# Optimization experiments

Hardware: AMD Instinct MI355X
Metric: run time of the kernel (lower is better)

Reference implementation:

```python
import jax, jax.numpy as jnp
import numpy as np

N, M, B = 1024, 8192, 8192  # W: [N, M], x: [B, N]
BLOCK = 32


def activation_quant(x):
    # per-tensor symmetric int8 fake-quant with STE
    scale = 127.0 / jnp.clip(jnp.max(jnp.abs(x)), 1e-8, None)
    x_q = jnp.clip(jnp.round(x * scale), -128.0, 127.0) / scale
    return x + jax.lax.stop_gradient(x_q - x)


def weight_quant_q2_k(w, block_size=BLOCK):
    # blockwise 2-bit quant with top-2 outliers kept at 4-bit, STE
    shape = w.shape
    wf = w.reshape(-1)
    n = wf.shape[0]
    pad = (-n) % block_size
    wf = jnp.pad(wf, (0, pad))
    blocks = wf.reshape(-1, block_size)
    scales = jnp.clip(jnp.max(jnp.abs(blocks), axis=1, keepdims=True), 1e-8, None)
    nb = blocks / scales
    k = min(2, block_size)
    _, top_idx = jax.lax.top_k(jnp.abs(nb), k)
    rows = jnp.arange(nb.shape[0])[:, None]
    top_mask = jnp.zeros(nb.shape, dtype=bool).at[rows, top_idx].set(True)
    q4 = jnp.round(nb * 7.0) / 7.0
    abs_nb = jnp.abs(nb)
    q2 = jnp.sign(nb) * jnp.where(abs_nb > 0.66, 1.0, 1.0 / 3.0)
    q = jnp.where(top_mask, q4, q2) * scales
    w_q = q.reshape(-1)[:n].reshape(shape)
    return w + jax.lax.stop_gradient(w_q - w)


def setup_inputs() -> dict:
    key = jax.random.key(0)
    k1, k2, k3 = jax.random.split(key, 3)
    x = jax.random.normal(k1, (B, N), dtype=jnp.float32)
    W = jax.random.normal(k2, (N, M), dtype=jnp.float32) / np.float32(np.sqrt(M))
    b = jax.random.normal(k3, (N,), dtype=jnp.float32)
    idx = jnp.arange(M // 2, dtype=jnp.int32)            # expanded (quantized) columns
    idx_comp = jnp.arange(M // 2, M, dtype=jnp.int32)    # continuous columns
    return {"x": x, "W": W, "b": b, "idx": idx, "idx_comp": idx_comp}


def reference(x, W, b, idx, idx_comp):
    W_exp_q = weight_quant_q2_k(jnp.take(W, idx, axis=1))   # [N, M/2]
    W_cont = jnp.take(W, idx_comp, axis=1)                  # [N, M/2]
    hidden_exp = activation_quant(x) @ W_exp_q              # [B, M/2]
    hidden_cont = x @ W_cont                                # [B, M/2]
    hidden = (jnp.zeros((x.shape[0], M), dtype=x.dtype)
              .at[:, idx].set(hidden_exp)
              .at[:, idx_comp].set(hidden_cont))            # scatter back to [B, M]
    h_exp = activation_quant(hidden[:, idx])
    out = jax.nn.relu(h_exp @ W_exp_q.T + hidden[:, idx_comp] @ W_cont.T + b)
    return out
```

## Files before the change

kernel.cpp:

```cpp
#include <hip/hip_runtime.h>
#include <hip/hip_bf16.h>
#include <cstdint>


using bf16x8 = __attribute__((ext_vector_type(8))) __bf16;
using f32x4  = __attribute__((ext_vector_type(4))) float;

typedef const __attribute__((address_space(1))) void g_void;
typedef __attribute__((address_space(3))) void l_void;

__device__ __forceinline__ void gload16(const void* g, void* l) {
  __builtin_amdgcn_global_load_lds((g_void*)g, (l_void*)l, 16, 0, 0);
}

__device__ __forceinline__ ushort f2bf(float f) {
  union { float f; unsigned u; } c; c.f = f;
  unsigned r = c.u + 0x7FFFu + ((c.u >> 16) & 1u);
  return (ushort)(r >> 16);
}
__device__ __forceinline__ float bf2f(ushort u) {
  union { unsigned u; float f; } c; c.u = ((unsigned)u) << 16;
  return c.f;
}

__global__ void prep_wa_kernel(const float* __restrict__ W,
                               const float4* __restrict__ x,
                               ushort* __restrict__ Wq,
                               ushort* __restrict__ WqT,
                               ushort* __restrict__ Wcb,
                               unsigned* __restrict__ amax_bits) {
  const int bidx = blockIdx.x;
  const int tid = threadIdx.x;

  if (bidx < 1024) {
    __shared__ __align__(16) ushort tile[64][72];
    const int rt = bidx >> 6;
    const int ct = bidx & 63;
    const int r0 = rt * 64, c0 = ct * 64;
    const int e = tid & 31;
    const int hw = tid >> 5;
    #pragma unroll
    for (int it = 0; it < 16; ++it) {
      const int g = it * 8 + hw;
      const int row = g >> 1;
      const int cg = (g & 1) * 32;
      const float w = W[(size_t)(r0 + row) * 8192 + c0 + cg + e];
      float aw = fabsf(w);
      float m = aw;
      #pragma unroll
      for (int d = 1; d <= 16; d <<= 1) m = fmaxf(m, __shfl_xor(m, d));
      int idx = (aw == m) ? e : 32;
      #pragma unroll
      for (int d = 1; d <= 16; d <<= 1) idx = min(idx, __shfl_xor(idx, d));
      const int i1 = idx;
      float a2 = (e == i1) ? -1.f : aw;
      float m2 = a2;
      #pragma unroll
      for (int d = 1; d <= 16; d <<= 1) m2 = fmaxf(m2, __shfl_xor(m2, d));
      int idx2 = (a2 == m2) ? e : 32;
      #pragma unroll
      for (int d = 1; d <= 16; d <<= 1) idx2 = min(idx2, __shfl_xor(idx2, d));
      const int i2 = idx2;

      const float scale = fmaxf(m, 1e-8f);
      const float nb = w / scale;
      float q;
      if (e == i1 || e == i2) {
        q = rintf(nb * 7.f) / 7.f;
      } else {
        float s = (nb > 0.f) ? 1.f : ((nb < 0.f) ? -1.f : 0.f);
        q = s * ((fabsf(nb) > 0.66f) ? 1.f : (1.f / 3.f));
      }
      const ushort qb = f2bf(q * scale);
      Wq[(size_t)(r0 + row) * 4096 + c0 + cg + e] = qb;
      tile[cg + e][row] = qb;
    }
    __syncthreads();
    const int c = tid >> 2;
    const int q4 = (tid & 3) * 16;
    uint4 v0 = *(const uint4*)&tile[c][q4];
    uint4 v1 = *(const uint4*)&tile[c][q4 + 8];
    *(uint4*)(WqT + (size_t)(c0 + c) * 1024 + r0 + q4) = v0;
    *(uint4*)(WqT + (size_t)(c0 + c) * 1024 + r0 + q4 + 8) = v1;
  } else if (bidx < 5120) {
    const int u = (bidx - 1024) * 256 + tid;
    const int row = u >> 10;
    const int c4 = u & 1023;
    float4 v = *(const float4*)(W + (size_t)row * 8192 + 4096 + c4 * 4);
    ushort4 o;
    o.x = f2bf(v.x); o.y = f2bf(v.y); o.z = f2bf(v.z); o.w = f2bf(v.w);
    *(ushort4*)(Wcb + (size_t)row * 4096 + c4 * 4) = o;
  } else {
    float m = 0.f;
    const int base = (bidx - 5120) * 256 + tid;
    const int stride = 2048 * 256;
    for (int i = base; i < 8192 * 1024 / 4; i += stride) {
      float4 v = x[i];
      m = fmaxf(m, fmaxf(fmaxf(fabsf(v.x), fabsf(v.y)),
                         fmaxf(fabsf(v.z), fabsf(v.w))));
    }
    #pragma unroll
    for (int off = 32; off > 0; off >>= 1) m = fmaxf(m, __shfl_down(m, off));
    __shared__ float wm[4];
    int lane = tid & 63, wave = tid >> 6;
    if (lane == 0) wm[wave] = m;
    __syncthreads();
    if (tid == 0) {
      float r = fmaxf(fmaxf(wm[0], wm[1]), fmaxf(wm[2], wm[3]));
      atomicMax(amax_bits, __float_as_uint(r));
    }
  }
}

__global__ void prep_x_kernel(const float4* __restrict__ x,
                              const unsigned* __restrict__ amax_bits,
                              uint4* __restrict__ xq, uint4* __restrict__ xbf) {
  const float amax = fmaxf(__uint_as_float(*amax_bits), 1e-8f);
  const float scale = 127.f / amax;
  const int base = blockIdx.x * 256 + threadIdx.x;
  const int stride = 2048 * 256;
  const int n8 = 8192 * 1024 / 8;
  for (int i = base; i < n8; i += stride) {
    float4 a = x[i * 2], b = x[i * 2 + 1];
    float v[8] = {a.x, a.y, a.z, a.w, b.x, b.y, b.z, b.w};
    unsigned qw[4], bw[4];
    #pragma unroll
    for (int j = 0; j < 4; ++j) {
      float q0 = fminf(fmaxf(rintf(v[2 * j] * scale), -128.f), 127.f) / scale;
      float q1 = fminf(fmaxf(rintf(v[2 * j + 1] * scale), -128.f), 127.f) / scale;
      qw[j] = (unsigned)f2bf(q0) | ((unsigned)f2bf(q1) << 16);
      bw[j] = (unsigned)f2bf(v[2 * j]) | ((unsigned)f2bf(v[2 * j + 1]) << 16);
    }
    xq[i] = make_uint4(qw[0], qw[1], qw[2], qw[3]);
    xbf[i] = make_uint4(bw[0], bw[1], bw[2], bw[3]);
  }
}

__global__ __launch_bounds__(256, 2) void gemm1_kernel(
    const ushort* __restrict__ Wcb,
    ushort* __restrict__ G,
    const ushort* __restrict__ Aq, const ushort* __restrict__ BT,
    ushort* __restrict__ Hexp, unsigned* __restrict__ amax_bits) {
  __shared__ __align__(16) ushort As[2][128 * 32];
  __shared__ __align__(16) ushort Bs[2][128 * 32];
  __shared__ float wredmax[4];

  const int bidx = blockIdx.x;
  const int tid = threadIdx.x;
  const int lane = tid & 63, wave = tid >> 6;
  const int l15 = lane & 15, quad = lane >> 4;
  const int wm = (wave >> 1) << 6, wn = (wave & 1) << 6;
  const int sel = (quad ^ ((l15 >> 1) & 3)) * 8;
  const int scs = ((tid & 3) ^ ((tid >> 3) & 3)) * 8;

  ushort* Asl0 = As[0] + tid * 8; ushort* Asl1 = As[1] + tid * 8;
  ushort* Bsl0 = Bs[0] + tid * 8; ushort* Bsl1 = Bs[1] + tid * 8;

  f32x4 acc[4][4];
  #pragma unroll
  for (int i = 0; i < 4; ++i)
    #pragma unroll
    for (int j = 0; j < 4; ++j) acc[i][j] = (f32x4){0.f, 0.f, 0.f, 0.f};

  if (bidx < 64) {
    const int gy = bidx >> 3, gx = bidx & 7;
    const int i0 = gy * 128, j0 = gx * 128;
    const ushort* Ag = Wcb + (size_t)(i0 + (tid >> 2)) * 4096 + scs;
    const ushort* Bg = Wcb + (size_t)(j0 + (tid >> 2)) * 4096 + scs;
    for (int k0 = 0; k0 < 4096; k0 += 64) {
      __syncthreads();
      gload16(Ag + k0, Asl0);
      gload16(Ag + (size_t)64 * 4096 + k0, Asl0 + 64 * 32);
      gload16(Bg + k0, Bsl0);
      gload16(Bg + (size_t)64 * 4096 + k0, Bsl0 + 64 * 32);
      gload16(Ag + k0 + 32, Asl1);
      gload16(Ag + (size_t)64 * 4096 + k0 + 32, Asl1 + 64 * 32);
      gload16(Bg + k0 + 32, Bsl1);
      gload16(Bg + (size_t)64 * 4096 + k0 + 32, Bsl1 + 64 * 32);
      __syncthreads();
      #pragma unroll
      for (int p = 0; p < 2; ++p) {
        bf16x8 af[4], bfr[4];
        #pragma unroll
        for (int i = 0; i < 4; ++i)
          af[i] = *(const bf16x8*)&As[p][(wm + i * 16 + l15) * 32 + sel];
        #pragma unroll
        for (int j = 0; j < 4; ++j)
          bfr[j] = *(const bf16x8*)&Bs[p][(wn + j * 16 + l15) * 32 + sel];
        #pragma unroll
        for (int i = 0; i < 4; ++i)
          #pragma unroll
          for (int j = 0; j < 4; ++j)
            acc[i][j] = __builtin_amdgcn_mfma_f32_16x16x32_bf16(af[i], bfr[j], acc[i][j], 0, 0, 0);
      }
    }
    const int row0 = i0 + wm + quad * 4;
    const int col0 = j0 + wn + l15;
    #pragma unroll
    for (int i = 0; i < 4; ++i)
      #pragma unroll
      for (int j = 0; j < 4; ++j)
        #pragma unroll
        for (int r = 0; r < 4; ++r)
          G[(size_t)(row0 + i * 16 + r) * 1024 + (col0 + j * 16)] = f2bf(acc[i][j][r]);
    return;
  }

  const int l = bidx - 64;
  const int xcd = l & 7;
  const int s = l >> 3;
  const int t = (xcd << 2) | (s >> 6);
  const int u = s & 63;
  const int bx = ((t & 3) << 3) | (u & 7);
  const int by = ((t >> 2) << 3) | (u >> 3);

  const ushort* Ag = Aq + (size_t)(by * 128 + (tid >> 2)) * 1024 + scs;
  const ushort* Bg = BT + (size_t)(bx * 128 + (tid >> 2)) * 1024 + scs;

  for (int k0 = 0; k0 < 1024; k0 += 64) {
    __syncthreads();
    gload16(Ag + k0, Asl0);
    gload16(Ag + 64 * 1024 + k0, Asl0 + 64 * 32);
    gload16(Bg + k0, Bsl0);
    gload16(Bg + 64 * 1024 + k0, Bsl0 + 64 * 32);
    gload16(Ag + k0 + 32, Asl1);
    gload16(Ag + 64 * 1024 + k0 + 32, Asl1 + 64 * 32);
    gload16(Bg + k0 + 32, Bsl1);
    gload16(Bg + 64 * 1024 + k0 + 32, Bsl1 + 64 * 32);
    __syncthreads();

    #pragma unroll
    for (int p = 0; p < 2; ++p) {
      bf16x8 af[4], bfr[4];
      #pragma unroll
      for (int i = 0; i < 4; ++i)
        af[i] = *(const bf16x8*)&As[p][(wm + i * 16 + l15) * 32 + sel];
      #pragma unroll
      for (int j = 0; j < 4; ++j)
        bfr[j] = *(const bf16x8*)&Bs[p][(wn + j * 16 + l15) * 32 + sel];
      #pragma unroll
      for (int i = 0; i < 4; ++i)
        #pragma unroll
        for (int j = 0; j < 4; ++j)
          acc[i][j] = __builtin_amdgcn_mfma_f32_16x16x32_bf16(af[i], bfr[j], acc[i][j], 0, 0, 0);
    }
  }

  const int row0 = by * 128 + wm + quad * 4;
  const int col0 = bx * 128 + wn + l15;
  float lmax = 0.f;
  #pragma unroll
  for (int i = 0; i < 4; ++i)
    #pragma unroll
    for (int j = 0; j < 4; ++j)
      #pragma unroll
      for (int r = 0; r < 4; ++r) {
        float v = acc[i][j][r];
        lmax = fmaxf(lmax, fabsf(v));
        Hexp[(size_t)(row0 + i * 16 + r) * 4096 + (col0 + j * 16)] = f2bf(v);
      }

  #pragma unroll
  for (int off = 32; off > 0; off >>= 1)
    lmax = fmaxf(lmax, __shfl_down(lmax, off));
  if (lane == 0) wredmax[wave] = lmax;
  __syncthreads();
  if (tid == 0) {
    float m = fmaxf(fmaxf(wredmax[0], wredmax[1]), fmaxf(wredmax[2], wredmax[3]));
    atomicMax(amax_bits, __float_as_uint(m));
  }
}

__global__ void quant_h_kernel(ushort* __restrict__ H,
                               const unsigned* __restrict__ amax_bits) {
  const float amax = fmaxf(__uint_as_float(*amax_bits), 1e-8f);
  const float scale = 127.f / amax;
  const int n8 = 8192 * 4096 / 8;
  for (int i = blockIdx.x * blockDim.x + threadIdx.x; i < n8;
       i += gridDim.x * blockDim.x) {
    uint4* p = (uint4*)H + i;
    uint4 a = *p;
    unsigned w[4] = {a.x, a.y, a.z, a.w};
    #pragma unroll
    for (int j = 0; j < 4; ++j) {
      float lo = bf2f((ushort)(w[j] & 0xFFFF));
      float hi = bf2f((ushort)(w[j] >> 16));
      lo = fminf(fmaxf(rintf(lo * scale), -128.f), 127.f) / scale;
      hi = fminf(fmaxf(rintf(hi * scale), -128.f), 127.f) / scale;
      w[j] = (unsigned)f2bf(lo) | ((unsigned)f2bf(hi) << 16);
    }
    *p = make_uint4(w[0], w[1], w[2], w[3]);
  }
}

__global__ __launch_bounds__(256, 2) void gemm2_kernel(
    const ushort* __restrict__ Hq, const ushort* __restrict__ Wq,
    const ushort* __restrict__ Xb, const ushort* __restrict__ G,
    const float* __restrict__ bias, float* __restrict__ out) {
  __shared__ __align__(16) ushort As[2][128 * 32];
  __shared__ __align__(16) ushort Bs[2][128 * 32];

  const int l = blockIdx.x;
  const int xcd = l & 7;
  const int s = l >> 3;
  const int by = (xcd << 3) | (s >> 3);
  const int bx = s & 7;

  const int tid = threadIdx.x;
  const int lane = tid & 63, wave = tid >> 6;
  const int wm = (wave >> 1) << 6, wn = (wave & 1) << 6;
  const int l15 = lane & 15, quad = lane >> 4;
  const int sel = (quad ^ ((l15 >> 1) & 3)) * 8;
  const int scs = ((tid & 3) ^ ((tid >> 3) & 3)) * 8;

  ushort* Asl0 = As[0] + tid * 8; ushort* Asl1 = As[1] + tid * 8;
  ushort* Bsl0 = Bs[0] + tid * 8; ushort* Bsl1 = Bs[1] + tid * 8;

  f32x4 acc[4][4];
  #pragma unroll
  for (int i = 0; i < 4; ++i)
    #pragma unroll
    for (int j = 0; j < 4; ++j) acc[i][j] = (f32x4){0.f, 0.f, 0.f, 0.f};

  {
    const ushort* Ag = Hq + (size_t)(by * 128 + (tid >> 2)) * 4096 + scs;
    const ushort* Bg = Wq + (size_t)(bx * 128 + (tid >> 2)) * 4096 + scs;
    for (int k0 = 0; k0 < 4096; k0 += 64) {
      __syncthreads();
      gload16(Ag + k0, Asl0);
      gload16(Ag + (size_t)64 * 4096 + k0, Asl0 + 64 * 32);
      gload16(Bg + k0, Bsl0);
      gload16(Bg + (size_t)64 * 4096 + k0, Bsl0 + 64 * 32);
      gload16(Ag + k0 + 32, Asl1);
      gload16(Ag + (size_t)64 * 4096 + k0 + 32, Asl1 + 64 * 32);
      gload16(Bg + k0 + 32, Bsl1);
      gload16(Bg + (size_t)64 * 4096 + k0 + 32, Bsl1 + 64 * 32);
      __syncthreads();
      #pragma unroll
      for (int p = 0; p < 2; ++p) {
        bf16x8 af[4], bfr[4];
        #pragma unroll
        for (int i = 0; i < 4; ++i)
          af[i] = *(const bf16x8*)&As[p][(wm + i * 16 + l15) * 32 + sel];
        #pragma unroll
        for (int j = 0; j < 4; ++j)
          bfr[j] = *(const bf16x8*)&Bs[p][(wn + j * 16 + l15) * 32 + sel];
        #pragma unroll
        for (int i = 0; i < 4; ++i)
          #pragma unroll
          for (int j = 0; j < 4; ++j)
            acc[i][j] = __builtin_amdgcn_mfma_f32_16x16x32_bf16(af[i], bfr[j], acc[i][j], 0, 0, 0);
      }
    }
  }
  {
    const ushort* Ag = Xb + (size_t)(by * 128 + (tid >> 2)) * 1024 + scs;
    const ushort* Bg = G + (size_t)(bx * 128 + (tid >> 2)) * 1024 + scs;
    for (int k0 = 0; k0 < 1024; k0 += 64) {
      __syncthreads();
      gload16(Ag + k0, Asl0);
      gload16(Ag + 64 * 1024 + k0, Asl0 + 64 * 32);
      gload16(Bg + k0, Bsl0);
      gload16(Bg + 64 * 1024 + k0, Bsl0 + 64 * 32);
      gload16(Ag + k0 + 32, Asl1);
      gload16(Ag + 64 * 1024 + k0 + 32, Asl1 + 64 * 32);
      gload16(Bg + k0 + 32, Bsl1);
      gload16(Bg + 64 * 1024 + k0 + 32, Bsl1 + 64 * 32);
      __syncthreads();
      #pragma unroll
      for (int p = 0; p < 2; ++p) {
        bf16x8 af[4], bfr[4];
        #pragma unroll
        for (int i = 0; i < 4; ++i)
          af[i] = *(const bf16x8*)&As[p][(wm + i * 16 + l15) * 32 + sel];
        #pragma unroll
        for (int j = 0; j < 4; ++j)
          bfr[j] = *(const bf16x8*)&Bs[p][(wn + j * 16 + l15) * 32 + sel];
        #pragma unroll
        for (int i = 0; i < 4; ++i)
          #pragma unroll
          for (int j = 0; j < 4; ++j)
            acc[i][j] = __builtin_amdgcn_mfma_f32_16x16x32_bf16(af[i], bfr[j], acc[i][j], 0, 0, 0);
      }
    }
  }

  const int row0 = by * 128 + wm + quad * 4;
  const int col0 = bx * 128 + wn + l15;
  #pragma unroll
  for (int i = 0; i < 4; ++i)
    #pragma unroll
    for (int j = 0; j < 4; ++j) {
      float bv = bias[col0 + j * 16];
      #pragma unroll
      for (int r = 0; r < 4; ++r) {
        float v = acc[i][j][r] + bv;
        v = fmaxf(v, 0.f);
        out[(size_t)(row0 + i * 16 + r) * 1024 + (col0 + j * 16)] = v;
      }
    }
}

extern "C" void kernel_launch(void* const* d_in, const int* in_sizes, int n_in,
                              void* d_out, int out_size, void* d_ws, size_t ws_size,
                              hipStream_t stream) {
  (void)in_sizes; (void)n_in; (void)out_size; (void)ws_size;
  const float* x = (const float*)d_in[0];
  const float* W = (const float*)d_in[1];
  const float* b = (const float*)d_in[2];

  char* ws = (char*)d_ws;
  unsigned* scal = (unsigned*)ws;
  ushort* xq   = (ushort*)(ws + 256);
  ushort* xbf  = xq   + (size_t)8192 * 1024;
  ushort* Wq   = xbf  + (size_t)8192 * 1024;
  ushort* WqT  = Wq   + (size_t)1024 * 4096;
  ushort* Wcb  = WqT  + (size_t)4096 * 1024;
  ushort* G    = Wcb  + (size_t)1024 * 4096;
  ushort* Hexp = G    + (size_t)1024 * 1024;

  hipMemsetAsync(scal, 0, 256, stream);
  prep_wa_kernel<<<7168, 256, 0, stream>>>(W, (const float4*)x, Wq, WqT, Wcb, scal);
  prep_x_kernel<<<2048, 256, 0, stream>>>((const float4*)x, scal,
                                          (uint4*)xq, (uint4*)xbf);
  gemm1_kernel<<<2112, 256, 0, stream>>>(Wcb, G, xq, WqT, Hexp, scal + 1);
  quant_h_kernel<<<4096, 256, 0, stream>>>(Hexp, scal + 1);
  gemm2_kernel<<<512, 256, 0, stream>>>(Hexp, Wq, xbf, G, b, (float*)d_out);
}
```

Before: 341.5 us.

## Fuse hidden activation quant into gemm2 A-load and drop memset via per-block amax slots

Removes the separate quant_h pass over the 8192x4096 bf16 hidden matrix. gemm2 now loads A tiles into registers, quantizes them through a 256-entry LDS dequant table, and writes them to LDS, with register prefetch of the next tile. This replaces the async global_load_lds path for A. The x amax reduction now writes per-block slots that prep_x reduces, and prep_wa zeros the gemm1 amax, so the memset launch goes away. Costs are extra VALU work and LDS traffic inside the GEMM main loop, plus synchronous register loads for A.

Result: no change. 347.3 us (+1.7%).

```diff
diff --git a/kernel.cpp b/kernel.cpp
--- a/kernel.cpp
+++ b/kernel.cpp
@@ -28,7 +28,7 @@
                                ushort* __restrict__ Wq,
                                ushort* __restrict__ WqT,
                                ushort* __restrict__ Wcb,
-                               unsigned* __restrict__ amax_bits) {
+                               unsigned* __restrict__ scal) {
   const int bidx = blockIdx.x;
   const int tid = threadIdx.x;
 
@@ -107,15 +107,24 @@
     __syncthreads();
     if (tid == 0) {
       float r = fmaxf(fmaxf(wm[0], wm[1]), fmaxf(wm[2], wm[3]));
-      atomicMax(amax_bits, __float_as_uint(r));
+      ((float*)(scal + 16))[bidx - 5120] = r;
+      if (bidx == 5120) scal[1] = 0u;
     }
   }
 }
 
 __global__ void prep_x_kernel(const float4* __restrict__ x,
-                              const unsigned* __restrict__ amax_bits,
+                              const float* __restrict__ slots,
                               uint4* __restrict__ xq, uint4* __restrict__ xbf) {
-  const float amax = fmaxf(__uint_as_float(*amax_bits), 1e-8f);
+  __shared__ float red[4];
+  float mm = 0.f;
+  for (int i = threadIdx.x; i < 2048; i += 256) mm = fmaxf(mm, slots[i]);
+  #pragma unroll
+  for (int off = 32; off > 0; off >>= 1) mm = fmaxf(mm, __shfl_down(mm, off));
+  if ((threadIdx.x & 63) == 0) red[threadIdx.x >> 6] = mm;
+  __syncthreads();
+  const float amax = fmaxf(fmaxf(fmaxf(red[0], red[1]), fmaxf(red[2], red[3])),
+                           1e-8f);
   const float scale = 127.f / amax;
   const int base = blockIdx.x * 256 + threadIdx.x;
   const int stride = 2048 * 256;
@@ -271,34 +280,14 @@
   }
 }
 
-__global__ void quant_h_kernel(ushort* __restrict__ H,
-                               const unsigned* __restrict__ amax_bits) {
-  const float amax = fmaxf(__uint_as_float(*amax_bits), 1e-8f);
-  const float scale = 127.f / amax;
-  const int n8 = 8192 * 4096 / 8;
-  for (int i = blockIdx.x * blockDim.x + threadIdx.x; i < n8;
-       i += gridDim.x * blockDim.x) {
-    uint4* p = (uint4*)H + i;
-    uint4 a = *p;
-    unsigned w[4] = {a.x, a.y, a.z, a.w};
-    #pragma unroll
-    for (int j = 0; j < 4; ++j) {
-      float lo = bf2f((ushort)(w[j] & 0xFFFF));
-      float hi = bf2f((ushort)(w[j] >> 16));
-      lo = fminf(fmaxf(rintf(lo * scale), -128.f), 127.f) / scale;
-      hi = fminf(fmaxf(rintf(hi * scale), -128.f), 127.f) / scale;
-      w[j] = (unsigned)f2bf(lo) | ((unsigned)f2bf(hi) << 16);
-    }
-    *p = make_uint4(w[0], w[1], w[2], w[3]);
-  }
-}
-
 __global__ __launch_bounds__(256, 2) void gemm2_kernel(
-    const ushort* __restrict__ Hq, const ushort* __restrict__ Wq,
+    const ushort* __restrict__ Hexp, const ushort* __restrict__ Wq,
     const ushort* __restrict__ Xb, const ushort* __restrict__ G,
-    const float* __restrict__ bias, float* __restrict__ out) {
+    const float* __restrict__ bias, const unsigned* __restrict__ amax_bits,
+    float* __restrict__ out) {
   __shared__ __align__(16) ushort As[2][128 * 32];
   __shared__ __align__(16) ushort Bs[2][128 * 32];
+  __shared__ ushort dq[256];
 
   const int l = blockIdx.x;
   const int xcd = l & 7;
@@ -313,6 +302,10 @@
   const int sel = (quad ^ ((l15 >> 1) & 3)) * 8;
   const int scs = ((tid & 3) ^ ((tid >> 3) & 3)) * 8;
 
+  const float amax = fmaxf(__uint_as_float(*amax_bits), 1e-8f);
+  const float scale = 127.f / amax;
+  dq[tid] = f2bf((float)(tid - 128) / scale);
+
   ushort* Asl0 = As[0] + tid * 8; ushort* Asl1 = As[1] + tid * 8;
   ushort* Bsl0 = Bs[0] + tid * 8; ushort* Bsl1 = Bs[1] + tid * 8;
 
@@ -323,19 +316,46 @@
     for (int j = 0; j < 4; ++j) acc[i][j] = (f32x4){0.f, 0.f, 0.f, 0.f};
 
   {
-    const ushort* Ag = Hq + (size_t)(by * 128 + (tid >> 2)) * 4096 + scs;
+    const ushort* Ag = Hexp + (size_t)(by * 128 + (tid >> 2)) * 4096 + scs;
     const ushort* Bg = Wq + (size_t)(bx * 128 + (tid >> 2)) * 4096 + scs;
+
+    auto quant8 = [&](uint4 a) -> uint4 {
+      unsigned w[4] = {a.x, a.y, a.z, a.w};
+      unsigned r[4];
+      #pragma unroll
+      for (int j = 0; j < 4; ++j) {
+        float lo = bf2f((ushort)(w[j] & 0xFFFF));
+        float hi = bf2f((ushort)(w[j] >> 16));
+        int il = (int)fminf(fmaxf(rintf(lo * scale), -128.f), 127.f) + 128;
+        int ih = (int)fminf(fmaxf(rintf(hi * scale), -128.f), 127.f) + 128;
+        r[j] = (unsigned)dq[il] | ((unsigned)dq[ih] << 16);
+      }
+      return make_uint4(r[0], r[1], r[2], r[3]);
+    };
+
+    uint4 a00, a01, a10, a11;
+    a00 = *(const uint4*)(Ag);
+    a01 = *(const uint4*)(Ag + 32);
+    a10 = *(const uint4*)(Ag + (size_t)64 * 4096);
+    a11 = *(const uint4*)(Ag + (size_t)64 * 4096 + 32);
+
     for (int k0 = 0; k0 < 4096; k0 += 64) {
       __syncthreads();
-      gload16(Ag + k0, Asl0);
-      gload16(Ag + (size_t)64 * 4096 + k0, Asl0 + 64 * 32);
+      *(uint4*)(Asl0)           = quant8(a00);
+      *(uint4*)(Asl1)           = quant8(a01);
+      *(uint4*)(Asl0 + 64 * 32) = quant8(a10);
+      *(uint4*)(Asl1 + 64 * 32) = quant8(a11);
       gload16(Bg + k0, Bsl0);
       gload16(Bg + (size_t)64 * 4096 + k0, Bsl0 + 64 * 32);
-      gload16(Ag + k0 + 32, Asl1);
-      gload16(Ag + (size_t)64 * 4096 + k0 + 32, Asl1 + 64 * 32);
       gload16(Bg + k0 + 32, Bsl1);
       gload16(Bg + (size_t)64 * 4096 + k0 + 32, Bsl1 + 64 * 32);
       __syncthreads();
+      if (k0 + 64 < 4096) {
+        a00 = *(const uint4*)(Ag + k0 + 64);
+        a01 = *(const uint4*)(Ag + k0 + 96);
+        a10 = *(const uint4*)(Ag + (size_t)64 * 4096 + k0 + 64);
+        a11 = *(const uint4*)(Ag + (size_t)64 * 4096 + k0 + 96);
+      }
       #pragma unroll
       for (int p = 0; p < 2; ++p) {
         bf16x8 af[4], bfr[4];
@@ -411,7 +431,7 @@
 
   char* ws = (char*)d_ws;
   unsigned* scal = (unsigned*)ws;
-  ushort* xq   = (ushort*)(ws + 256);
+  ushort* xq   = (ushort*)(ws + 16384);
   ushort* xbf  = xq   + (size_t)8192 * 1024;
   ushort* Wq   = xbf  + (size_t)8192 * 1024;
   ushort* WqT  = Wq   + (size_t)1024 * 4096;
@@ -419,11 +439,11 @@
   ushort* G    = Wcb  + (size_t)1024 * 4096;
   ushort* Hexp = G    + (size_t)1024 * 1024;
 
-  hipMemsetAsync(scal, 0, 256, stream);
   prep_wa_kernel<<<7168, 256, 0, stream>>>(W, (const float4*)x, Wq, WqT, Wcb, scal);
-  prep_x_kernel<<<2048, 256, 0, stream>>>((const float4*)x, scal,
+  prep_x_kernel<<<2048, 256, 0, stream>>>((const float4*)x,
+                                          (const float*)(scal + 16),
                                           (uint4*)xq, (uint4*)xbf);
   gemm1_kernel<<<2112, 256, 0, stream>>>(Wcb, G, xq, WqT, Hexp, scal + 1);
-  quant_h_kernel<<<4096, 256, 0, stream>>>(Hexp, scal + 1);
-  gemm2_kernel<<<512, 256, 0, stream>>>(Hexp, Wq, xbf, G, b, (float*)d_out);
-}
+  gemm2_kernel<<<512, 256, 0, stream>>>(Hexp, Wq, xbf, G, b, scal + 1,
+                                        (float*)d_out);
+}
```

## Switch GEMMs to 32x32x16 MFMA tiles and drop memset via per-block amax slots

Applied to the files above, without the earlier changes.

All GEMM inner loops move from 16x16x32 bf16 MFMA with 4x4 accumulators to 32x32x16 MFMA with 2x2 accumulators of 16 floats, with matching LDS fragment addressing and epilogue index mapping. The larger MFMA shape needs fewer LDS fragment reads per flop and fewer instructions. Separately, the x abs-max reduction now writes per-block partials to workspace slots that each prep_x block reduces itself, and scal[1] is zeroed inside the kernel. This removes the hipMemsetAsync launch and the global atomic, at the cost of every prep_x block redundantly reducing 2048 slots.

Result: slower. 351.4 us (+2.9%).

```diff
diff --git a/kernel.cpp b/kernel.cpp
--- a/kernel.cpp
+++ b/kernel.cpp
@@ -4,7 +4,7 @@
 
 
 using bf16x8 = __attribute__((ext_vector_type(8))) __bf16;
-using f32x4  = __attribute__((ext_vector_type(4))) float;
+using f32x16 = __attribute__((ext_vector_type(16))) float;
 
 typedef const __attribute__((address_space(1))) void g_void;
 typedef __attribute__((address_space(3))) void l_void;
@@ -28,7 +28,7 @@
                                ushort* __restrict__ Wq,
                                ushort* __restrict__ WqT,
                                ushort* __restrict__ Wcb,
-                               unsigned* __restrict__ amax_bits) {
+                               unsigned* __restrict__ scal) {
   const int bidx = blockIdx.x;
   const int tid = threadIdx.x;
 
@@ -107,15 +107,24 @@
     __syncthreads();
     if (tid == 0) {
       float r = fmaxf(fmaxf(wm[0], wm[1]), fmaxf(wm[2], wm[3]));
-      atomicMax(amax_bits, __float_as_uint(r));
+      ((float*)(scal + 16))[bidx - 5120] = r;
+      if (bidx == 5120) scal[1] = 0u;
     }
   }
 }
 
 __global__ void prep_x_kernel(const float4* __restrict__ x,
-                              const unsigned* __restrict__ amax_bits,
+                              const float* __restrict__ slots,
                               uint4* __restrict__ xq, uint4* __restrict__ xbf) {
-  const float amax = fmaxf(__uint_as_float(*amax_bits), 1e-8f);
+  __shared__ float red[4];
+  float mm = 0.f;
+  for (int i = threadIdx.x; i < 2048; i += 256) mm = fmaxf(mm, slots[i]);
+  #pragma unroll
+  for (int off = 32; off > 0; off >>= 1) mm = fmaxf(mm, __shfl_down(mm, off));
+  if ((threadIdx.x & 63) == 0) red[threadIdx.x >> 6] = mm;
+  __syncthreads();
+  const float amax = fmaxf(fmaxf(fmaxf(red[0], red[1]), fmaxf(red[2], red[3])),
+                           1e-8f);
   const float scale = 127.f / amax;
   const int base = blockIdx.x * 256 + threadIdx.x;
   const int stride = 2048 * 256;
@@ -136,6 +145,7 @@
   }
 }
 
+
 __global__ __launch_bounds__(256, 2) void gemm1_kernel(
     const ushort* __restrict__ Wcb,
     ushort* __restrict__ G,
@@ -148,19 +158,21 @@
   const int bidx = blockIdx.x;
   const int tid = threadIdx.x;
   const int lane = tid & 63, wave = tid >> 6;
-  const int l15 = lane & 15, quad = lane >> 4;
+  const int l31 = lane & 31, hi = lane >> 5;
   const int wm = (wave >> 1) << 6, wn = (wave & 1) << 6;
-  const int sel = (quad ^ ((l15 >> 1) & 3)) * 8;
+  const int swz = (l31 >> 1) & 3;
   const int scs = ((tid & 3) ^ ((tid >> 3) & 3)) * 8;
 
   ushort* Asl0 = As[0] + tid * 8; ushort* Asl1 = As[1] + tid * 8;
   ushort* Bsl0 = Bs[0] + tid * 8; ushort* Bsl1 = Bs[1] + tid * 8;
 
-  f32x4 acc[4][4];
-  #pragma unroll
-  for (int i = 0; i < 4; ++i)
-    #pragma unroll
-    for (int j = 0; j < 4; ++j) acc[i][j] = (f32x4){0.f, 0.f, 0.f, 0.f};
+  f32x16 acc[2][2];
+  #pragma unroll
+  for (int i = 0; i < 2; ++i)
+    #pragma unroll
+    for (int j = 0; j < 2; ++j)
+      #pragma unroll
+      for (int r = 0; r < 16; ++r) acc[i][j][r] = 0.f;
 
   if (bidx < 64) {
     const int gy = bidx >> 3, gx = bidx & 7;
@@ -180,29 +192,39 @@
       __syncthreads();
       #pragma unroll
       for (int p = 0; p < 2; ++p) {
-        bf16x8 af[4], bfr[4];
-        #pragma unroll
-        for (int i = 0; i < 4; ++i)
-          af[i] = *(const bf16x8*)&As[p][(wm + i * 16 + l15) * 32 + sel];
-        #pragma unroll
-        for (int j = 0; j < 4; ++j)
-          bfr[j] = *(const bf16x8*)&Bs[p][(wn + j * 16 + l15) * 32 + sel];
-        #pragma unroll
-        for (int i = 0; i < 4; ++i)
-          #pragma unroll
-          for (int j = 0; j < 4; ++j)
-            acc[i][j] = __builtin_amdgcn_mfma_f32_16x16x32_bf16(af[i], bfr[j], acc[i][j], 0, 0, 0);
-      }
-    }
-    const int row0 = i0 + wm + quad * 4;
-    const int col0 = j0 + wn + l15;
-    #pragma unroll
-    for (int i = 0; i < 4; ++i)
-      #pragma unroll
-      for (int j = 0; j < 4; ++j)
-        #pragma unroll
-        for (int r = 0; r < 4; ++r)
-          G[(size_t)(row0 + i * 16 + r) * 1024 + (col0 + j * 16)] = f2bf(acc[i][j][r]);
+        bf16x8 af[2][2], bfr[2][2];
+        #pragma unroll
+        for (int i = 0; i < 2; ++i)
+          #pragma unroll
+          for (int ks = 0; ks < 2; ++ks)
+            af[i][ks] = *(const bf16x8*)&As[p][(wm + i * 32 + l31) * 32 +
+                                              (((ks * 2 + hi) ^ swz) * 8)];
+        #pragma unroll
+        for (int j = 0; j < 2; ++j)
+          #pragma unroll
+          for (int ks = 0; ks < 2; ++ks)
+            bfr[j][ks] = *(const bf16x8*)&Bs[p][(wn + j * 32 + l31) * 32 +
+                                               (((ks * 2 + hi) ^ swz) * 8)];
+        #pragma unroll
+        for (int ks = 0; ks < 2; ++ks)
+          #pragma unroll
+          for (int i = 0; i < 2; ++i)
+            #pragma unroll
+            for (int j = 0; j < 2; ++j)
+              acc[i][j] = __builtin_amdgcn_mfma_f32_32x32x16_bf16(
+                  af[i][ks], bfr[j][ks], acc[i][j], 0, 0, 0);
+      }
+    }
+    #pragma unroll
+    for (int i = 0; i < 2; ++i)
+      #pragma unroll
+      for (int j = 0; j < 2; ++j)
+        #pragma unroll
+        for (int r = 0; r < 16; ++r) {
+          const int row = i0 + wm + i * 32 + (r & 3) + 8 * (r >> 2) + 4 * hi;
+          const int col = j0 + wn + j * 32 + l31;
+          G[(size_t)row * 1024 + col] = f2bf(acc[i][j][r]);
+        }
     return;
   }
 
@@ -231,33 +253,42 @@
 
     #pragma unroll
     for (int p = 0; p < 2; ++p) {
-      bf16x8 af[4], bfr[4];
-      #pragma unroll
-      for (int i = 0; i < 4; ++i)
-        af[i] = *(const bf16x8*)&As[p][(wm + i * 16 + l15) * 32 + sel];
-      #pragma unroll
-      for (int j = 0; j < 4; ++j)
-        bfr[j] = *(const bf16x8*)&Bs[p][(wn + j * 16 + l15) * 32 + sel];
-      #pragma unroll
-      for (int i = 0; i < 4; ++i)
-        #pragma unroll
-        for (int j = 0; j < 4; ++j)
-          acc[i][j] = __builtin_amdgcn_mfma_f32_16x16x32_bf16(af[i], bfr[j], acc[i][j], 0, 0, 0);
-    }
-  }
-
-  const int row0 = by * 128 + wm + quad * 4;
-  const int col0 = bx * 128 + wn + l15;
+      bf16x8 af[2][2], bfr[2][2];
+      #pragma unroll
+      for (int i = 0; i < 2; ++i)
+        #pragma unroll
+        for (int ks = 0; ks < 2; ++ks)
+          af[i][ks] = *(const bf16x8*)&As[p][(wm + i * 32 + l31) * 32 +
+                                            (((ks * 2 + hi) ^ swz) * 8)];
+      #pragma unroll
+      for (int j = 0; j < 2; ++j)
+        #pragma unroll
+        for (int ks = 0; ks < 2; ++ks)
+          bfr[j][ks] = *(const bf16x8*)&Bs[p][(wn + j * 32 + l31) * 32 +
+                                             (((ks * 2 + hi) ^ swz) * 8)];
+      #pragma unroll
+      for (int ks = 0; ks < 2; ++ks)
+        #pragma unroll
+        for (int i = 0; i < 2; ++i)
+          #pragma unroll
+          for (int j = 0; j < 2; ++j)
+            acc[i][j] = __builtin_amdgcn_mfma_f32_32x32x16_bf16(
+                af[i][ks], bfr[j][ks], acc[i][j], 0, 0, 0);
+    }
+  }
+
   float lmax = 0.f;
   #pragma unroll
-  for (int i = 0; i < 4; ++i)
-    #pragma unroll
-    for (int j = 0; j < 4; ++j)
-      #pragma unroll
-      for (int r = 0; r < 4; ++r) {
+  for (int i = 0; i < 2; ++i)
+    #pragma unroll
+    for (int j = 0; j < 2; ++j)
+      #pragma unroll
+      for (int r = 0; r < 16; ++r) {
+        const int row = by * 128 + wm + i * 32 + (r & 3) + 8 * (r >> 2) + 4 * hi;
+        const int col = bx * 128 + wn + j * 32 + l31;
         float v = acc[i][j][r];
         lmax = fmaxf(lmax, fabsf(v));
-        Hexp[(size_t)(row0 + i * 16 + r) * 4096 + (col0 + j * 16)] = f2bf(v);
+        Hexp[(size_t)row * 4096 + col] = f2bf(v);
       }
 
   #pragma unroll
@@ -309,18 +340,20 @@
   const int tid = threadIdx.x;
   const int lane = tid & 63, wave = tid >> 6;
   const int wm = (wave >> 1) << 6, wn = (wave & 1) << 6;
-  const int l15 = lane & 15, quad = lane >> 4;
-  const int sel = (quad ^ ((l15 >> 1) & 3)) * 8;
+  const int l31 = lane & 31, hi = lane >> 5;
+  const int swz = (l31 >> 1) & 3;
   const int scs = ((tid & 3) ^ ((tid >> 3) & 3)) * 8;
 
   ushort* Asl0 = As[0] + tid * 8; ushort* Asl1 = As[1] + tid * 8;
   ushort* Bsl0 = Bs[0] + tid * 8; ushort* Bsl1 = Bs[1] + tid * 8;
 
-  f32x4 acc[4][4];
-  #pragma unroll
-  for (int i = 0; i < 4; ++i)
-    #pragma unroll
-    for (int j = 0; j < 4; ++j) acc[i][j] = (f32x4){0.f, 0.f, 0.f, 0.f};
+  f32x16 acc[2][2];
+  #pragma unroll
+  for (int i = 0; i < 2; ++i)
+    #pragma unroll
+    for (int j = 0; j < 2; ++j)
+      #pragma unroll
+      for (int r = 0; r < 16; ++r) acc[i][j][r] = 0.f;
 
   {
     const ushort* Ag = Hq + (size_t)(by * 128 + (tid >> 2)) * 4096 + scs;
@@ -338,18 +371,27 @@
       __syncthreads();
       #pragma unroll
       for (int p = 0; p < 2; ++p) {
-        bf16x8 af[4], bfr[4];
-        #pragma unroll
-        for (int i = 0; i < 4; ++i)
-          af[i] = *(const bf16x8*)&As[p][(wm + i * 16 + l15) * 32 + sel];
-        #pragma unroll
-        for (int j = 0; j < 4; ++j)
-          bfr[j] = *(const bf16x8*)&Bs[p][(wn + j * 16 + l15) * 32 + sel];
-        #pragma unroll
-        for (int i = 0; i < 4; ++i)
-          #pragma unroll
-          for (int j = 0; j < 4; ++j)
-            acc[i][j] = __builtin_amdgcn_mfma_f32_16x16x32_bf16(af[i], bfr[j], acc[i][j], 0, 0, 0);
+        bf16x8 af[2][2], bfr[2][2];
+        #pragma unroll
+        for (int i = 0; i < 2; ++i)
+          #pragma unroll
+          for (int ks = 0; ks < 2; ++ks)
+            af[i][ks] = *(const bf16x8*)&As[p][(wm + i * 32 + l31) * 32 +
+                                              (((ks * 2 + hi) ^ swz) * 8)];
+        #pragma unroll
+        for (int j = 0; j < 2; ++j)
+          #pragma unroll
+          for (int ks = 0; ks < 2; ++ks)
+            bfr[j][ks] = *(const bf16x8*)&Bs[p][(wn + j * 32 + l31) * 32 +
+                                               (((ks * 2 + hi) ^ swz) * 8)];
+        #pragma unroll
+        for (int ks = 0; ks < 2; ++ks)
+          #pragma unroll
+          for (int i = 0; i < 2; ++i)
+            #pragma unroll
+            for (int j = 0; j < 2; ++j)
+              acc[i][j] = __builtin_amdgcn_mfma_f32_32x32x16_bf16(
+                  af[i][ks], bfr[j][ks], acc[i][j], 0, 0, 0);
       }
     }
   }
@@ -369,34 +411,43 @@
       __syncthreads();
       #pragma unroll
       for (int p = 0; p < 2; ++p) {
-        bf16x8 af[4], bfr[4];
-        #pragma unroll
-        for (int i = 0; i < 4; ++i)
-          af[i] = *(const bf16x8*)&As[p][(wm + i * 16 + l15) * 32 + sel];
-        #pragma unroll
-        for (int j = 0; j < 4; ++j)
-          bfr[j] = *(const bf16x8*)&Bs[p][(wn + j * 16 + l15) * 32 + sel];
-        #pragma unroll
-        for (int i = 0; i < 4; ++i)
-          #pragma unroll
-          for (int j = 0; j < 4; ++j)
-            acc[i][j] = __builtin_amdgcn_mfma_f32_16x16x32_bf16(af[i], bfr[j], acc[i][j], 0, 0, 0);
-      }
-    }
-  }
-
-  const int row0 = by * 128 + wm + quad * 4;
-  const int col0 = bx * 128 + wn + l15;
-  #pragma unroll
-  for (int i = 0; i < 4; ++i)
-    #pragma unroll
-    for (int j = 0; j < 4; ++j) {
-      float bv = bias[col0 + j * 16];
-      #pragma unroll
-      for (int r = 0; r < 4; ++r) {
+        bf16x8 af[2][2], bfr[2][2];
+        #pragma unroll
+        for (int i = 0; i < 2; ++i)
+          #pragma unroll
+          for (int ks = 0; ks < 2; ++ks)
+            af[i][ks] = *(const bf16x8*)&As[p][(wm + i * 32 + l31) * 32 +
+                                              (((ks * 2 + hi) ^ swz) * 8)];
+        #pragma unroll
+        for (int j = 0; j < 2; ++j)
+          #pragma unroll
+          for (int ks = 0; ks < 2; ++ks)
+            bfr[j][ks] = *(const bf16x8*)&Bs[p][(wn + j * 32 + l31) * 32 +
+                                               (((ks * 2 + hi) ^ swz) * 8)];
+        #pragma unroll
+        for (int ks = 0; ks < 2; ++ks)
+          #pragma unroll
+          for (int i = 0; i < 2; ++i)
+            #pragma unroll
+            for (int j = 0; j < 2; ++j)
+              acc[i][j] = __builtin_amdgcn_mfma_f32_32x32x16_bf16(
+                  af[i][ks], bfr[j][ks], acc[i][j], 0, 0, 0);
+      }
+    }
+  }
+
+  #pragma unroll
+  for (int i = 0; i < 2; ++i)
+    #pragma unroll
+    for (int j = 0; j < 2; ++j) {
+      const int col = bx * 128 + wn + j * 32 + l31;
+      const float bv = bias[col];
+      #pragma unroll
+      for (int r = 0; r < 16; ++r) {
+        const int row = by * 128 + wm + i * 32 + (r & 3) + 8 * (r >> 2) + 4 * hi;
         float v = acc[i][j][r] + bv;
         v = fmaxf(v, 0.f);
-        out[(size_t)(row0 + i * 16 + r) * 1024 + (col0 + j * 16)] = v;
+        out[(size_t)row * 1024 + col] = v;
       }
     }
 }
@@ -411,7 +462,7 @@
 
   char* ws = (char*)d_ws;
   unsigned* scal = (unsigned*)ws;
-  ushort* xq   = (ushort*)(ws + 256);
+  ushort* xq   = (ushort*)(ws + 16384);
   ushort* xbf  = xq   + (size_t)8192 * 1024;
   ushort* Wq   = xbf  + (size_t)8192 * 1024;
   ushort* WqT  = Wq   + (size_t)1024 * 4096;
@@ -419,9 +470,9 @@
   ushort* G    = Wcb  + (size_t)1024 * 4096;
   ushort* Hexp = G    + (size_t)1024 * 1024;
 
-  hipMemsetAsync(scal, 0, 256, stream);
   prep_wa_kernel<<<7168, 256, 0, stream>>>(W, (const float4*)x, Wq, WqT, Wcb, scal);
-  prep_x_kernel<<<2048, 256, 0, stream>>>((const float4*)x, scal,
+  prep_x_kernel<<<2048, 256, 0, stream>>>((const float4*)x,
+                                          (const float*)(scal + 16),
                                           (uint4*)xq, (uint4*)xbf);
   gemm1_kernel<<<2112, 256, 0, stream>>>(Wcb, G, xq, WqT, Hexp, scal + 1);
   quant_h_kernel<<<4096, 256, 0, stream>>>(Hexp, scal + 1);
```
